# Optimization experiments

Hardware: AMD Instinct MI355X
Metric: run time of the kernel (lower is better)

Reference implementation:

```python
import jax, jax.numpy as jnp
import numpy as np

D_EMB, D_HID, D_LAT, K = 512, 512, 256, 7
SEQ, BATCH = 512, 128


def setup_inputs() -> dict:
    key = jax.random.key(0)
    ks = jax.random.split(key, 10)
    x = jax.random.normal(ks[0], (SEQ, BATCH, D_EMB), jnp.float32)
    z = jax.random.normal(ks[1], (SEQ // 4, BATCH, D_LAT), jnp.float32)
    # Conv1d(d_latent, 2*d_hidden, K, groups=d_latent): weight [2*dh, 1, K]
    conv0_w = jax.random.normal(ks[2], (2 * D_HID, 1, K), jnp.float32) * 0.2
    conv0_b = jax.random.normal(ks[3], (2 * D_HID,), jnp.float32) * 0.1
    # Conv1d(d_hidden, 2*d_hidden, K, groups=d_hidden): weight [2*dh, 1, K]
    conv1_w = jax.random.normal(ks[4], (2 * D_HID, 1, K), jnp.float32) * 0.2
    conv1_b = jax.random.normal(ks[5], (2 * D_HID,), jnp.float32) * 0.1
    # LSTM(input=d_emb+d_hid, hidden=d_emb): gate order i,f,g,o
    gin = D_EMB + D_HID
    w_ih = jax.random.normal(ks[6], (4 * D_EMB, gin), jnp.float32) * (1.0 / np.sqrt(gin))
    w_hh = jax.random.normal(ks[7], (4 * D_EMB, D_EMB), jnp.float32) * (1.0 / np.sqrt(D_EMB))
    b_ih = jax.random.normal(ks[8], (4 * D_EMB,), jnp.float32) * 0.05
    b_hh = jax.random.normal(ks[9], (4 * D_EMB,), jnp.float32) * 0.05
    return {"x": x, "z": z, "conv0_w": conv0_w, "conv0_b": conv0_b,
            "conv1_w": conv1_w, "conv1_b": conv1_b,
            "w_ih": w_ih, "w_hh": w_hh, "b_ih": b_ih, "b_hh": b_hh}


def _upsample(z, w, b):
    # z: [L, B, Cin] -> depthwise-grouped conv + relu -> reshape doubles length
    zb = jnp.transpose(z, (1, 2, 0))  # [B, Cin, L]
    groups = zb.shape[1]              # groups = in_channels (weight I-dim is 1)
    pad = w.shape[-1] // 2
    y = jax.lax.conv_general_dilated(
        zb, w, window_strides=(1,), padding=[(pad, pad)],
        dimension_numbers=("NCH", "OIH", "NCH"), feature_group_count=groups)
    y = jax.nn.relu(y + b[None, :, None])          # [B, 2*dh, L]
    B, C2, L = y.shape
    y = jnp.transpose(y, (0, 2, 1)).reshape(B, 2 * L, C2 // 2)
    return jnp.transpose(y, (1, 0, 2))             # [2L, B, dh]


def reference(x, z, conv0_w, conv0_b, conv1_w, conv1_b, w_ih, w_hh, b_ih, b_hh):
    # eval mode: input/word dropout and weight dropout are identity
    z = _upsample(z, conv0_w, conv0_b)
    z = _upsample(z, conv1_w, conv1_b)   # [SEQ, B, d_hidden]
    inp = jnp.concatenate([x[:-1], z[1:]], axis=-1)  # [SEQ-1, B, d_emb+d_hid]
    # precompute input-to-gate projection across all timesteps
    gates_x = jnp.einsum("tbi,gi->tbg", inp, w_ih) + b_ih + b_hh
    H = w_hh.shape[1]
    B = inp.shape[1]

    def step(carry, gx):
        h, c = carry
        gates = gx + h @ w_hh.T
        i, f, g, o = jnp.split(gates, 4, axis=-1)
        c = jax.nn.sigmoid(f) * c + jax.nn.sigmoid(i) * jnp.tanh(g)
        h = jax.nn.sigmoid(o) * jnp.tanh(c)
        return (h, c), h

    h0 = jnp.zeros((B, H), inp.dtype)
    _, hs = jax.lax.scan(step, (h0, h0), gates_x)
    return hs  # [SEQ-1, B, d_embedding]
```

## Files before the change

kernel.cpp:

```cpp
#include <hip/hip_runtime.h>
#include <hip/hip_bf16.h>

typedef unsigned short u16;
typedef unsigned long long u64;
typedef short bf16x8 __attribute__((ext_vector_type(8)));
typedef float f32x4 __attribute__((ext_vector_type(4)));

__device__ __forceinline__ float ldbf(const u16* p) {
    __hip_bfloat16 h = *(const __hip_bfloat16*)p;
    return __bfloat162float(h);
}
__device__ __forceinline__ void stbf(u16* p, float f) {
    *(__hip_bfloat16*)p = __float2bfloat16(f);
}
__device__ __forceinline__ u16 f2bfu(float f) {
    __hip_bfloat16 h = __float2bfloat16(f);
    return *(u16*)&h;
}
__device__ __forceinline__ float bf2f(u16 v) {
    union { unsigned u; float f; } x; x.u = ((unsigned)v) << 16; return x.f;
}
__device__ __forceinline__ float sigm(float x) {
    return 1.0f / (1.0f + __expf(-x));
}
__device__ __forceinline__ float tanh_fast(float x) {
    float e = __expf(2.0f * x);
    return 1.0f - 2.0f / (e + 1.0f);
}

__global__ __launch_bounds__(256) void cvt_bf16(const float* __restrict__ in,
                                                u16* __restrict__ out, int n) {
    int i = blockIdx.x * 256 + threadIdx.x;
    if (i < n) stbf(out + i, in[i]);
}

template <bool INF32>
__global__ __launch_bounds__(256) void upsample(const void* __restrict__ in_,
                                                const float* __restrict__ w,
                                                const float* __restrict__ bias_,
                                                u16* __restrict__ out,
                                                int Lin, int shift) {
    const int Cin = 1024 >> shift;
    const int total = 2 * Lin * 128 * 512;
    int idx = blockIdx.x * 256 + threadIdx.x;
    if (idx >= total) return;
    const int c  = idx & 511;
    const int bb = (idx >> 9) & 127;
    const int tp = idx >> 16;
    const int s  = tp & 1;
    const int l  = tp >> 1;
    const int oc = c + (s << 9);
    const int ch = oc >> shift;
    float acc = bias_[oc];
    #pragma unroll
    for (int k = 0; k < 7; ++k) {
        int li = l + k - 3;
        if (li >= 0 && li < Lin) {
            size_t off = ((size_t)li * 128 + bb) * Cin + ch;
            float v = INF32 ? ((const float*)in_)[off] : ldbf((const u16*)in_ + off);
            acc += w[oc * 7 + k] * v;
        }
    }
    stbf(out + idx, fmaxf(acc, 0.0f));
}

__global__ __launch_bounds__(256) void gemm_gates(const float* __restrict__ x,
                                                  const u16* __restrict__ z2,
                                                  const float* __restrict__ wih,
                                                  const float* __restrict__ bih,
                                                  const float* __restrict__ bhh,
                                                  u16* __restrict__ gates) {
    __shared__ __align__(16) u16 smA[128 * 32];
    __shared__ __align__(16) u16 smB[128 * 32];
    const int tid  = threadIdx.x;
    const int lane = tid & 63;
    const int wave = tid >> 6;
    const int wm = wave >> 1, wn = wave & 1;
    const size_t mbase = (size_t)blockIdx.x * 128;
    const size_t nbase = (size_t)blockIdx.y * 128;

    f32x4 acc[4][4] = {};

    const int srow = tid >> 1;
    const int scol = (tid & 1) * 16;

    for (int kt = 0; kt < 32; ++kt) {
        const int kb = kt * 32;
        if (kb < 512) {
            const float* src = x + (mbase + srow) * 512 + kb + scol;
            alignas(16) u16 tmp[16];
            #pragma unroll
            for (int q = 0; q < 16; ++q) stbf(&tmp[q], src[q]);
            *(int4*)&smA[srow * 32 + scol]     = *(const int4*)&tmp[0];
            *(int4*)&smA[srow * 32 + scol + 8] = *(const int4*)&tmp[8];
        } else {
            const u16* src = z2 + 65536 + (mbase + srow) * 512 + (kb - 512) + scol;
            *(int4*)&smA[srow * 32 + scol]     = *(const int4*)(src);
            *(int4*)&smA[srow * 32 + scol + 8] = *(const int4*)(src + 8);
        }
        {
            const float* src = wih + (nbase + srow) * 1024 + kb + scol;
            alignas(16) u16 tmp[16];
            #pragma unroll
            for (int q = 0; q < 16; ++q) stbf(&tmp[q], src[q]);
            *(int4*)&smB[srow * 32 + scol]     = *(const int4*)&tmp[0];
            *(int4*)&smB[srow * 32 + scol + 8] = *(const int4*)&tmp[8];
        }
        __syncthreads();

        bf16x8 af[4], bfr[4];
        #pragma unroll
        for (int mi = 0; mi < 4; ++mi)
            af[mi] = *(const bf16x8*)&smA[(wm * 64 + mi * 16 + (lane & 15)) * 32 + (lane >> 4) * 8];
        #pragma unroll
        for (int ni = 0; ni < 4; ++ni)
            bfr[ni] = *(const bf16x8*)&smB[(wn * 64 + ni * 16 + (lane & 15)) * 32 + (lane >> 4) * 8];
        #pragma unroll
        for (int mi = 0; mi < 4; ++mi)
            #pragma unroll
            for (int ni = 0; ni < 4; ++ni)
                acc[mi][ni] = __builtin_amdgcn_mfma_f32_16x16x32_bf16(af[mi], bfr[ni], acc[mi][ni], 0, 0, 0);
        __syncthreads();
    }

    u16* gt = gates + (size_t)blockIdx.x * 262144;
    #pragma unroll
    for (int ni = 0; ni < 4; ++ni) {
        const int n = (int)nbase + wn * 64 + ni * 16 + (lane & 15);
        const float bias = bih[n] + bhh[n];
        const int g  = n >> 9;
        const int jh = n & 511;
        u16* gb = gt + (size_t)(jh >> 4) * 8192 + (size_t)(g * 16 + (jh & 15));
        #pragma unroll
        for (int mi = 0; mi < 4; ++mi) {
            const int b = wm * 64 + mi * 16 + (lane >> 4) * 4;
            #pragma unroll
            for (int r = 0; r < 4; ++r)
                stbf(gb + (size_t)(b + r) * 64, acc[mi][ni][r] + bias);
        }
    }
}

__global__ __launch_bounds__(256) void lstm_persist(const u16* __restrict__ gates,
                                                    const u16* __restrict__ whh,
                                                    u16* __restrict__ hbuf,
                                                    float* __restrict__ out,
                                                    unsigned* __restrict__ flags) {
    __shared__ __align__(16) u16 smW[32768];
    __shared__ __align__(16) u16 smH[16384];
    __shared__ __align__(16) float smG[4 * 32 * 18];

    const int tid  = threadIdx.x;
    const int lane = tid & 63;
    const int wave = tid >> 6;
    const int bid  = blockIdx.x;
    const int grp  = bid >> 5;
    const int jt   = bid & 31;
    const int b0   = grp << 5;
    const int jh0  = jt << 4;
    unsigned* myflag = flags + grp * 2048 + jt * 64;

    for (int i = tid; i < 4096; i += 256) {
        const int row = i >> 6;
        const int c8  = i & 63;
        const u16* src = whh + ((size_t)((row >> 4) * 512 + jh0 + (row & 15))) * 512 + c8 * 8;
        int4 v = *(const int4*)src;
        int byte = row * 1024 + c8 * 16;
        byte ^= (row & 7) << 4;
        *(int4*)((char*)smW + byte) = v;
    }

    const int fr = lane & 15;
    const int kq = lane >> 4;
    const int br = tid >> 3;
    const int j2 = (tid & 7) * 2;
    float cA = 0.0f, cB = 0.0f;

    __syncthreads();

    const int brow = wave * 16 + fr;
    const int bxor = (brow & 7) << 4;
    const int axor = (fr & 7) << 4;
    bf16x8 wfrag[16];
    #pragma unroll
    for (int kt = 0; kt < 16; ++kt)
        wfrag[kt] = *(const bf16x8*)((const char*)smW + ((brow * 1024 + kt * 64 + kq * 16) ^ bxor));

    for (int t = 0; t < 511; ++t) {
        const u64* hp = (const u64*)(hbuf + (size_t)(t & 1) * 65536 + (size_t)b0 * 512);
        u64 tmp[16];
        #pragma unroll
        for (int i = 0; i < 16; ++i)
            tmp[i] = __hip_atomic_load(hp + i * 256 + tid,
                                       __ATOMIC_RELAXED, __HIP_MEMORY_SCOPE_AGENT);
        __builtin_amdgcn_sched_barrier(0);
        #pragma unroll
        for (int i = 0; i < 16; ++i) {
            const int e   = i * 256 + tid;
            const int row = e >> 7;
            const int c4  = e & 127;
            const int byte = (row * 1024 + c4 * 8) ^ ((row & 7) << 4);
            *(u64*)((char*)smH + byte) = tmp[i];
        }
        const u16* gsrc = gates + (size_t)t * 262144 + (size_t)jt * 8192 + (size_t)b0 * 64;
        unsigned gx4[4];
        #pragma unroll
        for (int g = 0; g < 4; ++g)
            gx4[g] = *(const unsigned*)(gsrc + br * 64 + g * 16 + j2);

        __syncthreads();

        f32x4 acc0 = {}, acc1 = {};
        #pragma unroll
        for (int kt = 0; kt < 16; ++kt) {
            const int kb = kt * 64 + kq * 16;
            bf16x8 a0 = *(const bf16x8*)((const char*)smH + ((fr * 1024 + kb) ^ axor));
            bf16x8 a1 = *(const bf16x8*)((const char*)smH + (((16 + fr) * 1024 + kb) ^ axor));
            acc0 = __builtin_amdgcn_mfma_f32_16x16x32_bf16(a0, wfrag[kt], acc0, 0, 0, 0);
            acc1 = __builtin_amdgcn_mfma_f32_16x16x32_bf16(a1, wfrag[kt], acc1, 0, 0, 0);
        }

        #pragma unroll
        for (int r = 0; r < 4; ++r) {
            smG[(wave * 32 + kq * 4 + r) * 18 + fr]      = acc0[r];
            smG[(wave * 32 + 16 + kq * 4 + r) * 18 + fr] = acc1[r];
        }
        __syncthreads();

        u16*   hdst = hbuf + (size_t)((t + 1) & 1) * 65536;
        float* odst = out + ((size_t)t * 128 + b0 + br) * 512 + jh0;
        float hn0, hn1;
        {
            const float gi = smG[(0 * 32 + br) * 18 + j2] + bf2f((u16)(gx4[0] & 0xffff));
            const float gf = smG[(1 * 32 + br) * 18 + j2] + bf2f((u16)(gx4[1] & 0xffff));
            const float gg = smG[(2 * 32 + br) * 18 + j2] + bf2f((u16)(gx4[2] & 0xffff));
            const float go = smG[(3 * 32 + br) * 18 + j2] + bf2f((u16)(gx4[3] & 0xffff));
            cA = sigm(gf) * cA + sigm(gi) * tanh_fast(gg);
            hn0 = sigm(go) * tanh_fast(cA);
        }
        {
            const float gi = smG[(0 * 32 + br) * 18 + j2 + 1] + bf2f((u16)(gx4[0] >> 16));
            const float gf = smG[(1 * 32 + br) * 18 + j2 + 1] + bf2f((u16)(gx4[1] >> 16));
            const float gg = smG[(2 * 32 + br) * 18 + j2 + 1] + bf2f((u16)(gx4[2] >> 16));
            const float go = smG[(3 * 32 + br) * 18 + j2 + 1] + bf2f((u16)(gx4[3] >> 16));
            cB = sigm(gf) * cB + sigm(gi) * tanh_fast(gg);
            hn1 = sigm(go) * tanh_fast(cB);
        }
        {
            const unsigned hw = (unsigned)f2bfu(hn0) | ((unsigned)f2bfu(hn1) << 16);
            __hip_atomic_store((unsigned*)(hdst + (size_t)(b0 + br) * 512 + jh0 + j2),
                               hw, __ATOMIC_RELAXED, __HIP_MEMORY_SCOPE_AGENT);
        }
        *(float2*)(odst + j2) = make_float2(hn0, hn1);

        if (t < 510) {
            asm volatile("s_waitcnt vmcnt(0)" ::: "memory");
            __syncthreads();
            if (tid == 0)
                __hip_atomic_store(myflag, (unsigned)(t + 1),
                                   __ATOMIC_RELAXED, __HIP_MEMORY_SCOPE_AGENT);
            if (wave == 0) {
                const unsigned tgt = (unsigned)(t + 1);
                unsigned* fp = flags + grp * 2048 + lane * 64;
                int done = (lane >= 32 || lane == jt) ? 1 : 0;
                while (!__all(done)) {
                    if (!done)
                        done = (__hip_atomic_load(fp, __ATOMIC_RELAXED,
                                                  __HIP_MEMORY_SCOPE_AGENT) >= tgt);
                }
            }
            __syncthreads();
            asm volatile("" ::: "memory");
        }
    }
}

extern "C" void kernel_launch(void* const* d_in, const int* in_sizes, int n_in,
                              void* d_out, int out_size, void* d_ws, size_t ws_size,
                              hipStream_t stream) {
    const float* x   = (const float*)d_in[0];
    const float* z   = (const float*)d_in[1];
    const float* c0w = (const float*)d_in[2];
    const float* c0b = (const float*)d_in[3];
    const float* c1w = (const float*)d_in[4];
    const float* c1b = (const float*)d_in[5];
    const float* wih = (const float*)d_in[6];
    const float* whh = (const float*)d_in[7];
    const float* bih = (const float*)d_in[8];
    const float* bhh = (const float*)d_in[9];
    float* out = (float*)d_out;
    char* ws = (char*)d_ws;

    u16*      z1     = (u16*)(ws);
    u16*      z2     = (u16*)(ws + 33554432);
    u16*      gates  = (u16*)(ws + 100663296);
    unsigned* flags  = (unsigned*)(ws + 368574464);
    u16*      hbuf   = (u16*)(ws + 368836608);
    u16*      whh_bf = (u16*)(ws + 369098752);

    hipMemsetAsync(flags, 0, 32768, stream);
    hipMemsetAsync(hbuf, 0, 131072, stream);

    cvt_bf16<<<dim3(4096), 256, 0, stream>>>(whh, whh_bf, 1048576);

    upsample<true ><<<dim3(16777216 / 256), 256, 0, stream>>>(z,  c0w, c0b, z1, 128, 2);
    upsample<false><<<dim3(33554432 / 256), 256, 0, stream>>>(z1, c1w, c1b, z2, 256, 1);

    gemm_gates<<<dim3(511, 16), 256, 0, stream>>>(x, z2, wih, bih, bhh, gates);

    {
        const u16* gates_a = gates;
        const u16* whh_a   = whh_bf;
        u16*       hbuf_a  = hbuf;
        float*     out_a   = out;
        unsigned*  flags_a = flags;
        void* args[] = {&gates_a, &whh_a, &hbuf_a, &out_a, &flags_a};
        hipLaunchCooperativeKernel((void*)lstm_persist, dim3(128), dim3(256),
                                   args, 0, stream);
    }
}
```

Measured before the change: 3.123 ms.

## Replace LSTM flag barrier with timestep-tagged hidden-state words and prefetch gates

```diff
diff --git a/kernel.cpp b/kernel.cpp
--- a/kernel.cpp
+++ b/kernel.cpp
@@ -13,9 +13,9 @@
 __device__ __forceinline__ void stbf(u16* p, float f) {
     *(__hip_bfloat16*)p = __float2bfloat16(f);
 }
-__device__ __forceinline__ u16 f2bfu(float f) {
+__device__ __forceinline__ unsigned f2bfu(float f) {
     __hip_bfloat16 h = __float2bfloat16(f);
-    return *(u16*)&h;
+    return (unsigned)*(u16*)&h;
 }
 __device__ __forceinline__ float bf2f(u16 v) {
     union { unsigned u; float f; } x; x.u = ((unsigned)v) << 16; return x.f;
@@ -143,135 +143,134 @@
 
 __global__ __launch_bounds__(256) void lstm_persist(const u16* __restrict__ gates,
                                                     const u16* __restrict__ whh,
-                                                    u16* __restrict__ hbuf,
-                                                    float* __restrict__ out,
-                                                    unsigned* __restrict__ flags) {
-    __shared__ __align__(16) u16 smW[32768];
-    __shared__ __align__(16) u16 smH[16384];
-    __shared__ __align__(16) float smG[4 * 32 * 18];
+                                                    unsigned* __restrict__ hbuf,
+                                                    float* __restrict__ out) {
+    __shared__ __align__(16) u16 smH[16 * 512];
+    __shared__ __align__(16) float smG[4 * 16 * 33];
 
     const int tid  = threadIdx.x;
     const int lane = tid & 63;
     const int wave = tid >> 6;
     const int bid  = blockIdx.x;
-    const int grp  = bid >> 5;
-    const int jt   = bid & 31;
-    const int b0   = grp << 5;
-    const int jh0  = jt << 4;
-    unsigned* myflag = flags + grp * 2048 + jt * 64;
-
-    for (int i = tid; i < 4096; i += 256) {
-        const int row = i >> 6;
-        const int c8  = i & 63;
-        const u16* src = whh + ((size_t)((row >> 4) * 512 + jh0 + (row & 15))) * 512 + c8 * 8;
-        int4 v = *(const int4*)src;
-        int byte = row * 1024 + c8 * 16;
-        byte ^= (row & 7) << 4;
-        *(int4*)((char*)smW + byte) = v;
-    }
+    const int grp  = bid >> 4;
+    const int jt   = bid & 15;
+    const int b0   = grp << 4;
+    const int jh0  = jt << 5;
 
     const int fr = lane & 15;
     const int kq = lane >> 4;
-    const int br = tid >> 3;
-    const int j2 = (tid & 7) * 2;
+    const int br = tid >> 4;
+    const int j2 = (tid & 15) * 2;
+
+    bf16x8 wf0[16], wf1[16];
+    {
+        const int n0 = wave * 512 + jh0 + fr;
+        const int n1 = n0 + 16;
+        #pragma unroll
+        for (int kt = 0; kt < 16; ++kt) {
+            wf0[kt] = *(const bf16x8*)(whh + (size_t)n0 * 512 + kt * 32 + kq * 8);
+            wf1[kt] = *(const bf16x8*)(whh + (size_t)n1 * 512 + kt * 32 + kq * 8);
+        }
+    }
+
+    const size_t gxoff = (size_t)(jt * 2 + (j2 >> 4)) * 8192
+                       + (size_t)(b0 + br) * 64 + (j2 & 15);
+    unsigned gxn[4];
+    #pragma unroll
+    for (int g = 0; g < 4; ++g)
+        gxn[g] = *(const unsigned*)(gates + gxoff + g * 16);
+
     float cA = 0.0f, cB = 0.0f;
-
-    __syncthreads();
-
-    const int brow = wave * 16 + fr;
-    const int bxor = (brow & 7) << 4;
     const int axor = (fr & 7) << 4;
-    bf16x8 wfrag[16];
-    #pragma unroll
-    for (int kt = 0; kt < 16; ++kt)
-        wfrag[kt] = *(const bf16x8*)((const char*)smW + ((brow * 1024 + kt * 64 + kq * 16) ^ bxor));
 
     for (int t = 0; t < 511; ++t) {
-        const u64* hp = (const u64*)(hbuf + (size_t)(t & 1) * 65536 + (size_t)b0 * 512);
-        u64 tmp[16];
-        #pragma unroll
-        for (int i = 0; i < 16; ++i)
-            tmp[i] = __hip_atomic_load(hp + i * 256 + tid,
-                                       __ATOMIC_RELAXED, __HIP_MEMORY_SCOPE_AGENT);
-        __builtin_amdgcn_sched_barrier(0);
-        #pragma unroll
-        for (int i = 0; i < 16; ++i) {
-            const int e   = i * 256 + tid;
-            const int row = e >> 7;
-            const int c4  = e & 127;
-            const int byte = (row * 1024 + c4 * 8) ^ ((row & 7) << 4);
-            *(u64*)((char*)smH + byte) = tmp[i];
-        }
-        const u16* gsrc = gates + (size_t)t * 262144 + (size_t)jt * 8192 + (size_t)b0 * 64;
-        unsigned gx4[4];
-        #pragma unroll
-        for (int g = 0; g < 4; ++g)
-            gx4[g] = *(const unsigned*)(gsrc + br * 64 + g * 16 + j2);
-
+        unsigned gxc[4];
+        #pragma unroll
+        for (int g = 0; g < 4; ++g) gxc[g] = gxn[g];
+        {
+            const int tn = (t < 510) ? t + 1 : t;
+            const u16* gsrc = gates + (size_t)tn * 262144 + gxoff;
+            #pragma unroll
+            for (int g = 0; g < 4; ++g)
+                gxn[g] = *(const unsigned*)(gsrc + g * 16);
+        }
+
+        {
+            const u64* hp = (const u64*)(hbuf + (size_t)(t & 1) * 65536
+                                              + (size_t)b0 * 512);
+            const unsigned tg = (unsigned)t;
+            unsigned pend = 0xffffu;
+            do {
+                u64 v[16];
+                #pragma unroll
+                for (int i = 0; i < 16; ++i)
+                    if (pend & (1u << i))
+                        v[i] = __hip_atomic_load(hp + i * 256 + tid,
+                                                 __ATOMIC_RELAXED,
+                                                 __HIP_MEMORY_SCOPE_AGENT);
+                #pragma unroll
+                for (int i = 0; i < 16; ++i)
+                    if (pend & (1u << i)) {
+                        const unsigned lo = (unsigned)v[i];
+                        const unsigned hi = (unsigned)(v[i] >> 32);
+                        if (((lo >> 16) == tg) & ((hi >> 16) == tg)) {
+                            const int e2  = (i * 256 + tid) * 2;
+                            const int row = e2 >> 9;
+                            const int c   = e2 & 511;
+                            *(unsigned*)((char*)smH +
+                                ((row * 1024 + c * 2) ^ ((row & 7) << 4))) =
+                                (lo & 0xffffu) | (hi << 16);
+                            pend &= ~(1u << i);
+                        }
+                    }
+            } while (pend);
+        }
         __syncthreads();
 
         f32x4 acc0 = {}, acc1 = {};
         #pragma unroll
         for (int kt = 0; kt < 16; ++kt) {
-            const int kb = kt * 64 + kq * 16;
-            bf16x8 a0 = *(const bf16x8*)((const char*)smH + ((fr * 1024 + kb) ^ axor));
-            bf16x8 a1 = *(const bf16x8*)((const char*)smH + (((16 + fr) * 1024 + kb) ^ axor));
-            acc0 = __builtin_amdgcn_mfma_f32_16x16x32_bf16(a0, wfrag[kt], acc0, 0, 0, 0);
-            acc1 = __builtin_amdgcn_mfma_f32_16x16x32_bf16(a1, wfrag[kt], acc1, 0, 0, 0);
+            bf16x8 a = *(const bf16x8*)((const char*)smH +
+                        ((fr * 1024 + kt * 64 + kq * 16) ^ axor));
+            acc0 = __builtin_amdgcn_mfma_f32_16x16x32_bf16(a, wf0[kt], acc0, 0, 0, 0);
+            acc1 = __builtin_amdgcn_mfma_f32_16x16x32_bf16(a, wf1[kt], acc1, 0, 0, 0);
         }
 
         #pragma unroll
         for (int r = 0; r < 4; ++r) {
-            smG[(wave * 32 + kq * 4 + r) * 18 + fr]      = acc0[r];
-            smG[(wave * 32 + 16 + kq * 4 + r) * 18 + fr] = acc1[r];
+            smG[(wave * 16 + kq * 4 + r) * 33 + fr]      = acc0[r];
+            smG[(wave * 16 + kq * 4 + r) * 33 + 16 + fr] = acc1[r];
         }
         __syncthreads();
 
-        u16*   hdst = hbuf + (size_t)((t + 1) & 1) * 65536;
-        float* odst = out + ((size_t)t * 128 + b0 + br) * 512 + jh0;
         float hn0, hn1;
         {
-            const float gi = smG[(0 * 32 + br) * 18 + j2] + bf2f((u16)(gx4[0] & 0xffff));
-            const float gf = smG[(1 * 32 + br) * 18 + j2] + bf2f((u16)(gx4[1] & 0xffff));
-            const float gg = smG[(2 * 32 + br) * 18 + j2] + bf2f((u16)(gx4[2] & 0xffff));
-            const float go = smG[(3 * 32 + br) * 18 + j2] + bf2f((u16)(gx4[3] & 0xffff));
+            const float gi = smG[(0 * 16 + br) * 33 + j2] + bf2f((u16)(gxc[0] & 0xffff));
+            const float gf = smG[(1 * 16 + br) * 33 + j2] + bf2f((u16)(gxc[1] & 0xffff));
+            const float gg = smG[(2 * 16 + br) * 33 + j2] + bf2f((u16)(gxc[2] & 0xffff));
+            const float go = smG[(3 * 16 + br) * 33 + j2] + bf2f((u16)(gxc[3] & 0xffff));
             cA = sigm(gf) * cA + sigm(gi) * tanh_fast(gg);
             hn0 = sigm(go) * tanh_fast(cA);
         }
         {
-            const float gi = smG[(0 * 32 + br) * 18 + j2 + 1] + bf2f((u16)(gx4[0] >> 16));
-            const float gf = smG[(1 * 32 + br) * 18 + j2 + 1] + bf2f((u16)(gx4[1] >> 16));
-            const float gg = smG[(2 * 32 + br) * 18 + j2 + 1] + bf2f((u16)(gx4[2] >> 16));
-            const float go = smG[(3 * 32 + br) * 18 + j2 + 1] + bf2f((u16)(gx4[3] >> 16));
+            const float gi = smG[(0 * 16 + br) * 33 + j2 + 1] + bf2f((u16)(gxc[0] >> 16));
+            const float gf = smG[(1 * 16 + br) * 33 + j2 + 1] + bf2f((u16)(gxc[1] >> 16));
+            const float gg = smG[(2 * 16 + br) * 33 + j2 + 1] + bf2f((u16)(gxc[2] >> 16));
+            const float go = smG[(3 * 16 + br) * 33 + j2 + 1] + bf2f((u16)(gxc[3] >> 16));
             cB = sigm(gf) * cB + sigm(gi) * tanh_fast(gg);
             hn1 = sigm(go) * tanh_fast(cB);
         }
         {
-            const unsigned hw = (unsigned)f2bfu(hn0) | ((unsigned)f2bfu(hn1) << 16);
-            __hip_atomic_store((unsigned*)(hdst + (size_t)(b0 + br) * 512 + jh0 + j2),
-                               hw, __ATOMIC_RELAXED, __HIP_MEMORY_SCOPE_AGENT);
-        }
+            const unsigned tg1 = (unsigned)(t + 1) << 16;
+            const unsigned w0 = f2bfu(hn0) | tg1;
+            const unsigned w1 = f2bfu(hn1) | tg1;
+            unsigned* hb = hbuf + (size_t)((t + 1) & 1) * 65536
+                                + (size_t)(b0 + br) * 512 + jh0 + j2;
+            __hip_atomic_store((u64*)hb, (u64)w0 | ((u64)w1 << 32),
+                               __ATOMIC_RELAXED, __HIP_MEMORY_SCOPE_AGENT);
+        }
+        float* odst = out + ((size_t)t * 128 + b0 + br) * 512 + jh0;
         *(float2*)(odst + j2) = make_float2(hn0, hn1);
-
-        if (t < 510) {
-            asm volatile("s_waitcnt vmcnt(0)" ::: "memory");
-            __syncthreads();
-            if (tid == 0)
-                __hip_atomic_store(myflag, (unsigned)(t + 1),
-                                   __ATOMIC_RELAXED, __HIP_MEMORY_SCOPE_AGENT);
-            if (wave == 0) {
-                const unsigned tgt = (unsigned)(t + 1);
-                unsigned* fp = flags + grp * 2048 + lane * 64;
-                int done = (lane >= 32 || lane == jt) ? 1 : 0;
-                while (!__all(done)) {
-                    if (!done)
-                        done = (__hip_atomic_load(fp, __ATOMIC_RELAXED,
-                                                  __HIP_MEMORY_SCOPE_AGENT) >= tgt);
-                }
-            }
-            __syncthreads();
-            asm volatile("" ::: "memory");
-        }
     }
 }
 
@@ -294,12 +293,10 @@
     u16*      z1     = (u16*)(ws);
     u16*      z2     = (u16*)(ws + 33554432);
     u16*      gates  = (u16*)(ws + 100663296);
-    unsigned* flags  = (unsigned*)(ws + 368574464);
-    u16*      hbuf   = (u16*)(ws + 368836608);
+    unsigned* hbuf   = (unsigned*)(ws + 368574464);
     u16*      whh_bf = (u16*)(ws + 369098752);
 
-    hipMemsetAsync(flags, 0, 32768, stream);
-    hipMemsetAsync(hbuf, 0, 131072, stream);
+    hipMemsetAsync(hbuf, 0, 262144, stream);
 
     cvt_bf16<<<dim3(4096), 256, 0, stream>>>(whh, whh_bf, 1048576);
 
@@ -311,10 +308,9 @@
     {
         const u16* gates_a = gates;
         const u16* whh_a   = whh_bf;
-        u16*       hbuf_a  = hbuf;
+        unsigned*  hbuf_a  = hbuf;
         float*     out_a   = out;
-        unsigned*  flags_a = flags;
-        void* args[] = {&gates_a, &whh_a, &hbuf_a, &out_a, &flags_a};
+        void* args[] = {&gates_a, &whh_a, &hbuf_a, &out_a};
         hipLaunchCooperativeKernel((void*)lstm_persist, dim3(128), dim3(256),
                                    args, 0, stream);
     }
```

Result: slower. 3.230 ms (+3.4%).
